# Performance work log

Hardware: AMD Instinct MI355X
Metric: run time of the kernel (lower is better)

## Reference

```python
import jax, jax.numpy as jnp
import numpy as np

B, C, W, H = 1024, 1, 128, 128
NUM_IDS = 64
MARGIN = 0.3


def setup_inputs() -> dict:
    key = jax.random.key(0)
    k1, k2 = jax.random.split(key)
    inputs = jax.random.normal(k1, (B, C, W, H), dtype=jnp.float32)
    targets = jax.random.randint(k2, (B,), 0, NUM_IDS, dtype=jnp.int32)
    return {"inputs": inputs, "targets": targets}


def _dc_align(anchor, other):
    # Batched cross-attention alignment (DCModuleOptimized assumption):
    # modi = softmax(anchor @ other^T / sqrt(h)) @ other, per sample.
    h = anchor.shape[-1]
    scale = 1.0 / jnp.sqrt(jnp.asarray(h, anchor.dtype))
    att = jax.nn.softmax(jnp.einsum('bij,bkj->bik', anchor, other) * scale, axis=-1)
    return jnp.einsum('bik,bkj->bij', att, other)


def reference(inputs, targets):
    b, c, w, h = inputs.shape
    x = inputs.reshape(b, -1)                      # (n, d); requires c == 1 downstream
    n = b
    # Pairwise Euclidean distances, stable clamp as in torch code
    sq = jnp.sum(x * x, axis=1)                    # (n,)
    dist = sq[:, None] + sq[None, :] - 2.0 * (x @ x.T)
    dist = jnp.sqrt(jnp.clip(dist, 1e-12, None))   # (n, n)
    mask = targets[:, None] == targets[None, :]    # (n, n) same-identity mask
    # Vectorized hard mining (replaces the per-row Python loop)
    NEG = jnp.asarray(-1e30, dist.dtype)
    POS = jnp.asarray(1e30, dist.dtype)
    hp_idx = jnp.argmax(jnp.where(mask, dist, NEG), axis=1)   # hardest positive per row
    hn_idx = jnp.argmin(jnp.where(mask, POS, dist), axis=1)   # hardest negative per row
    anchor = x.reshape(b, w, h)
    h_pos = anchor[hp_idx]                         # (b, w, h) gathered hard positives
    h_neg = anchor[hn_idx]                         # (b, w, h) gathered hard negatives
    # DC module applied over the whole batch at once
    modi_pos = _dc_align(anchor, h_pos)
    modi_neg = _dc_align(anchor, h_neg)
    dap = anchor.reshape(b, -1) - modi_pos.reshape(b, -1)
    dan = anchor.reshape(b, -1) - modi_neg.reshape(b, -1)
    dist_ap = jnp.sqrt(jnp.sum(dap * dap, axis=1))
    dist_an = jnp.sqrt(jnp.sum(dan * dan, axis=1))
    # MarginRankingLoss with y = 1: mean(relu(dist_ap - dist_an + margin))
    loss = jnp.mean(jax.nn.relu(dist_ap - dist_an + MARGIN))
    return loss
```

## Files before the change

### kernel.cpp

```cpp
#include <hip/hip_runtime.h>
#include <stdint.h>

#define NSAMP 1024
#define D 16384
#define WH 128
#define MARGIN 0.3f
#define KS 8
#define KSUB (D / KS)
#define SCALE 0.08838834764831845f
#define RSCALE 11.313708498984761f

typedef unsigned int uint;
typedef unsigned short ushort_t;

typedef __attribute__((ext_vector_type(8))) short bf16x8;
typedef __attribute__((ext_vector_type(4))) float f32x4;

__device__ __forceinline__ float bf2f(unsigned short b) {
    return __uint_as_float(((uint)b) << 16);
}
__device__ __forceinline__ unsigned short f2bf(float f) {
    uint u = __float_as_uint(f);
    u += 0x7fffu + ((u >> 16) & 1u);
    return (unsigned short)(u >> 16);
}
__device__ __forceinline__ void gload_lds16(const void* g, void* l) {
    __builtin_amdgcn_global_load_lds(
        (const __attribute__((address_space(1))) uint32_t*)g,
        (__attribute__((address_space(3))) uint32_t*)l, 16, 0, 0);
}
__device__ __forceinline__ bf16x8 bf8_half(bf16x8 v) {
    union { bf16x8 b; uint u[4]; } c;
    c.b = v;
    c.u[0] -= 0x00800080u; c.u[1] -= 0x00800080u;
    c.u[2] -= 0x00800080u; c.u[3] -= 0x00800080u;
    return c.b;
}
__device__ __forceinline__ int lds_off(int row, int col) {
    return row * 256 + ((((col >> 3) ^ (row & 15)) << 4) | ((col & 7) << 1));
}

__global__ __launch_bounds__(256) void k_norms_split(const float* __restrict__ x,
                                                     float* __restrict__ sq,
                                                     ushort_t* __restrict__ xhi,
                                                     ushort_t* __restrict__ xlo) {
    int b = blockIdx.x;
    int tid = threadIdx.x;
    const float* xr = x + (size_t)b * D;
    ushort_t* hr = xhi + (size_t)b * D;
    ushort_t* lr = xlo + (size_t)b * D;
    float s = 0.f;
    #pragma unroll
    for (int m = 0; m < 16; ++m) {
        int e = m * 1024 + tid * 4;
        float4 v = *(const float4*)(xr + e);
        s += v.x * v.x + v.y * v.y + v.z * v.z + v.w * v.w;
        ushort4 h, l;
        h.x = f2bf(v.x); l.x = f2bf(v.x - bf2f(h.x));
        h.y = f2bf(v.y); l.y = f2bf(v.y - bf2f(h.y));
        h.z = f2bf(v.z); l.z = f2bf(v.z - bf2f(h.z));
        h.w = f2bf(v.w); l.w = f2bf(v.w - bf2f(h.w));
        *(ushort4*)(hr + e) = h;
        *(ushort4*)(lr + e) = l;
    }
    for (int off = 32; off; off >>= 1) s += __shfl_down(s, off, 64);
    __shared__ float red[4];
    if ((tid & 63) == 0) red[tid >> 6] = s;
    __syncthreads();
    if (tid == 0) sq[b] = red[0] + red[1] + red[2] + red[3];
}

__global__ __launch_bounds__(256) void k_gram_mfma(const ushort_t* __restrict__ xhi,
                                                   const ushort_t* __restrict__ xlo,
                                                   float* __restrict__ Gp) {
    int lin = blockIdx.x + 8 * blockIdx.y + 64 * blockIdx.z;
    int ks = lin & 7, bi = (lin >> 3) & 7, bj = lin >> 6;
    int i0 = bi * 128, j0 = bj * 128;
    int tid = threadIdx.x;
    int w = tid >> 6, lane = tid & 63;
    int wm = w & 1, wn = w >> 1;
    int quad = lane >> 4, m16 = lane & 15;
    int srow = lane >> 2, sseg = lane & 3;

    __shared__ __align__(16) ushort_t Ahi_s[128 * 32];
    __shared__ __align__(16) ushort_t Bhi_s[128 * 32];
    __shared__ __align__(16) ushort_t Blo_s[128 * 32];

    f32x4 acc[4][4];
    #pragma unroll
    for (int ii = 0; ii < 4; ++ii)
        #pragma unroll
        for (int jj = 0; jj < 4; ++jj)
            acc[ii][jj] = (f32x4){0.f, 0.f, 0.f, 0.f};

    const size_t Abase = (size_t)i0 * D;
    const size_t Bbase = (size_t)j0 * D;

    for (int kb = 0; kb < KSUB / 32; ++kb) {
        int k0 = ks * KSUB + kb * 32;
        #pragma unroll
        for (int c = 0; c < 2; ++c) {
            int r = w * 32 + c * 16 + srow;
            size_t go = (size_t)r * D + k0 + sseg * 8;
            int lo = (w * 32 + c * 16) * 32;
            gload_lds16(xhi + Abase + go, &Ahi_s[lo]);
            gload_lds16(xhi + Bbase + go, &Bhi_s[lo]);
            gload_lds16(xlo + Bbase + go, &Blo_s[lo]);
        }
        __syncthreads();

        bf16x8 ah[4], bh[4], bl[4];
        #pragma unroll
        for (int ii = 0; ii < 4; ++ii) {
            int ar = wm * 64 + ii * 16 + m16;
            ah[ii] = *(const bf16x8*)&Ahi_s[ar * 32 + quad * 8];
        }
        #pragma unroll
        for (int jj = 0; jj < 4; ++jj) {
            int br = wn * 64 + jj * 16 + m16;
            bh[jj] = *(const bf16x8*)&Bhi_s[br * 32 + quad * 8];
            bl[jj] = *(const bf16x8*)&Blo_s[br * 32 + quad * 8];
        }
        #pragma unroll
        for (int ii = 0; ii < 4; ++ii) {
            bf16x8 ahh = bf8_half(ah[ii]);
            #pragma unroll
            for (int jj = 0; jj < 4; ++jj) {
                acc[ii][jj] = __builtin_amdgcn_mfma_f32_16x16x32_bf16(ahh, bh[jj], acc[ii][jj], 0, 0, 0);
                acc[ii][jj] = __builtin_amdgcn_mfma_f32_16x16x32_bf16(ah[ii], bl[jj], acc[ii][jj], 0, 0, 0);
            }
        }
        __syncthreads();
    }

    float* Gb = Gp + (size_t)ks * NSAMP * NSAMP;
    #pragma unroll
    for (int ii = 0; ii < 4; ++ii)
        #pragma unroll
        for (int jj = 0; jj < 4; ++jj) {
            int rg = i0 + wm * 64 + ii * 16 + quad * 4;
            int cg = j0 + wn * 64 + jj * 16 + m16;
            #pragma unroll
            for (int r = 0; r < 4; ++r)
                Gb[(size_t)(rg + r) * NSAMP + cg] = acc[ii][jj][r];
        }
}

__global__ __launch_bounds__(256) void k_fold_sym(const float* __restrict__ Gp,
                                                  float* __restrict__ G) {
    int J = blockIdx.x, I = blockIdx.y;
    int t = threadIdx.x;
    int r = t >> 4, c4 = (t & 15) * 4;
    __shared__ float TJ[64][65];
    float4 sIJ[4];
    #pragma unroll
    for (int rr = 0; rr < 4; ++rr) {
        int row = rr * 16 + r;
        size_t oIJ = (size_t)(I * 64 + row) * NSAMP + J * 64 + c4;
        size_t oJI = (size_t)(J * 64 + row) * NSAMP + I * 64 + c4;
        float4 a = {0.f, 0.f, 0.f, 0.f}, bb = {0.f, 0.f, 0.f, 0.f};
        #pragma unroll
        for (int p = 0; p < KS; ++p) {
            float4 v = *(const float4*)(Gp + (size_t)p * NSAMP * NSAMP + oIJ);
            float4 w = *(const float4*)(Gp + (size_t)p * NSAMP * NSAMP + oJI);
            a.x += v.x; a.y += v.y; a.z += v.z; a.w += v.w;
            bb.x += w.x; bb.y += w.y; bb.z += w.z; bb.w += w.w;
        }
        sIJ[rr] = a;
        TJ[row][c4 + 0] = bb.x; TJ[row][c4 + 1] = bb.y;
        TJ[row][c4 + 2] = bb.z; TJ[row][c4 + 3] = bb.w;
    }
    __syncthreads();
    #pragma unroll
    for (int rr = 0; rr < 4; ++rr) {
        int row = rr * 16 + r;
        float4 v = sIJ[rr];
        v.x += TJ[c4 + 0][row]; v.y += TJ[c4 + 1][row];
        v.z += TJ[c4 + 2][row]; v.w += TJ[c4 + 3][row];
        *(float4*)(G + (size_t)(I * 64 + row) * NSAMP + J * 64 + c4) = v;
    }
}

__global__ void k_select(const float* __restrict__ G,
                         const float* __restrict__ sq, const int* __restrict__ tgt,
                         int* __restrict__ hp, int* __restrict__ hn,
                         float* __restrict__ dsq) {
    int i = blockIdx.x;
    int tid = threadIdx.x;
    float sqi = sq[i];
    int ti = tgt[i];
    float pv = -3.0e38f; int pj = 0x7FFFFFFF;
    float nv = 3.0e38f;  int nj = 0x7FFFFFFF;
    #pragma unroll
    for (int m = 0; m < 4; ++m) {
        int j = tid + 256 * m;
        float g = G[(size_t)i * NSAMP + j];
        float d2 = sqi + sq[j] - 2.f * g;
        float d = sqrtf(fmaxf(d2, 1e-12f));
        bool same = (tgt[j] == ti);
        float cp = same ? d : -1e30f;
        float cn = same ? 1e30f : d;
        if (cp > pv || (cp == pv && j < pj)) { pv = cp; pj = j; }
        if (cn < nv || (cn == nv && j < nj)) { nv = cn; nj = j; }
    }
    for (int off = 32; off; off >>= 1) {
        float opv = __shfl_down(pv, off, 64); int opj = __shfl_down(pj, off, 64);
        float onv = __shfl_down(nv, off, 64); int onj = __shfl_down(nj, off, 64);
        if (opv > pv || (opv == pv && opj < pj)) { pv = opv; pj = opj; }
        if (onv < nv || (onv == nv && onj < nj)) { nv = onv; nj = onj; }
    }
    __shared__ float spv[4], snv[4];
    __shared__ int spj[4], snj[4];
    if ((tid & 63) == 0) { int wv = tid >> 6; spv[wv] = pv; spj[wv] = pj; snv[wv] = nv; snj[wv] = nj; }
    __syncthreads();
    if (tid == 0) {
        for (int wv = 1; wv < 4; ++wv) {
            if (spv[wv] > pv || (spv[wv] == pv && spj[wv] < pj)) { pv = spv[wv]; pj = spj[wv]; }
            if (snv[wv] < nv || (snv[wv] == nv && snj[wv] < nj)) { nv = snv[wv]; nj = snj[wv]; }
        }
        hp[i] = pj; hn[i] = nj;
        dsq[i] = sqi; dsq[NSAMP + i] = sqi;
    }
}

__global__ __launch_bounds__(256) void k_dc_mfma(const ushort_t* __restrict__ xhi,
                                                 const int* __restrict__ hp,
                                                 const int* __restrict__ hn,
                                                 float* __restrict__ dsq) {
    int b = blockIdx.x;
    int which = blockIdx.y;
    int q = blockIdx.z;
    int oidx = (which == 0) ? hp[b] : hn[b];
    const ushort_t* Ag = xhi + (size_t)b * D;
    const ushort_t* Og = xhi + (size_t)oidx * D;

    __shared__ __align__(16) char smem[32768];

    int tid = threadIdx.x;
    int wv = tid >> 6, lane = tid & 63;
    int quad = lane >> 4, m16 = lane & 15;
    int rt = q * 4 + wv;

    bf16x8 af[4];
    #pragma unroll
    for (int ks = 0; ks < 4; ++ks)
        af[ks] = *(const bf16x8*)(Ag + (rt * 16 + m16) * WH + ks * 32 + quad * 8);

    {
        uint4 stg[8];
        #pragma unroll
        for (int k = 0; k < 8; ++k)
            stg[k] = *(const uint4*)((const char*)Og + (size_t)(tid + 256 * k) * 16);
        #pragma unroll
        for (int k = 0; k < 8; ++k) {
            int g = tid + 256 * k;
            *(uint4*)(smem + lds_off(g >> 4, (g & 15) * 8)) = stg[k];
        }
    }
    __syncthreads();

    f32x4 acc[8];
    #pragma unroll
    for (int ti = 0; ti < 8; ++ti)
        acc[ti] = (f32x4){0.f, 0.f, 0.f, 0.f};
    #pragma unroll
    for (int ks = 0; ks < 4; ++ks) {
        bf16x8 of[8];
        #pragma unroll
        for (int ti = 0; ti < 8; ++ti)
            of[ti] = *(const bf16x8*)(smem + lds_off(ti * 16 + m16, (ks * 4 + quad) * 8));
        #pragma unroll
        for (int ti = 0; ti < 8; ++ti)
            acc[ti] = __builtin_amdgcn_mfma_f32_16x16x32_bf16(of[ti], af[ks], acc[ti], 0, 0, 0);
    }

    int c0 = (tid & 31) * 4, h0 = (tid >> 5) * 16;
    uint4 trd[4][2];
    #pragma unroll
    for (int j = 0; j < 4; ++j)
        #pragma unroll
        for (int k = 0; k < 2; ++k)
            trd[j][k] = *(const uint4*)(smem + lds_off(c0 + j, h0 + 8 * k));
    __syncthreads();

    #pragma unroll
    for (int i = 0; i < 16; ++i) {
        uint v[4];
        #pragma unroll
        for (int j = 0; j < 4; ++j) {
            uint wo = ((const uint*)&trd[j][i >> 3])[(i >> 1) & 3];
            v[j] = (i & 1) ? (wo >> 16) : (wo & 0xffffu);
        }
        uint2 pk;
        pk.x = v[0] | (v[1] << 16);
        pk.y = v[2] | (v[3] << 16);
        *(uint2*)(smem + lds_off(h0 + i, c0)) = pk;
    }

    float tpart = 0.f;
    bf16x8 pf[4];
    {
        float mx = -3.0e38f;
        #pragma unroll
        for (int ti = 0; ti < 8; ++ti)
            #pragma unroll
            for (int r = 0; r < 4; ++r) {
                float s = acc[ti][r] * SCALE;
                acc[ti][r] = s;
                mx = fmaxf(mx, s);
            }
        mx = fmaxf(mx, __shfl_xor(mx, 16, 64));
        mx = fmaxf(mx, __shfl_xor(mx, 32, 64));
        float sum = 0.f, tnum = 0.f;
        #pragma unroll
        for (int ti = 0; ti < 8; ++ti)
            #pragma unroll
            for (int r = 0; r < 4; ++r) {
                float s = acc[ti][r];
                float e = __expf(s - mx);
                acc[ti][r] = e;
                sum += e;
                tnum += s * e;
            }
        sum += __shfl_xor(sum, 16, 64);
        sum += __shfl_xor(sum, 32, 64);
        tnum += __shfl_xor(tnum, 16, 64);
        tnum += __shfl_xor(tnum, 32, 64);
        float inv = 1.f / sum;
        tpart = 0.25f * tnum * inv;

        uint Ep[8][2];
        #pragma unroll
        for (int ti = 0; ti < 8; ++ti) {
            Ep[ti][0] = (uint)f2bf(acc[ti][0] * inv) |
                        ((uint)f2bf(acc[ti][1] * inv) << 16);
            Ep[ti][1] = (uint)f2bf(acc[ti][2] * inv) |
                        ((uint)f2bf(acc[ti][3] * inv) << 16);
        }
        int tih = quad >> 1;
        #pragma unroll
        for (int ks = 0; ks < 4; ++ks) {
            union { uint u[4]; bf16x8 v; } fr;
            #pragma unroll
            for (int k = 0; k < 4; ++k) {
                int src = (((quad << 1) + (k >> 1)) & 3) * 16 + m16;
                int a = __shfl((int)Ep[2 * ks + 0][k & 1], src, 64);
                int bsh = __shfl((int)Ep[2 * ks + 1][k & 1], src, 64);
                fr.u[k] = (uint)((tih == 0) ? a : bsh);
            }
            pf[ks] = fr.v;
        }
    }
    __syncthreads();

    #pragma unroll
    for (int tj = 0; tj < 8; ++tj)
        acc[tj] = (f32x4){0.f, 0.f, 0.f, 0.f};
    #pragma unroll
    for (int ks = 0; ks < 4; ++ks) {
        bf16x8 otf[8];
        #pragma unroll
        for (int tj = 0; tj < 8; ++tj)
            otf[tj] = *(const bf16x8*)(smem + lds_off(tj * 16 + m16, (ks * 4 + quad) * 8));
        #pragma unroll
        for (int tj = 0; tj < 8; ++tj)
            acc[tj] = __builtin_amdgcn_mfma_f32_16x16x32_bf16(pf[ks], otf[tj], acc[tj], 0, 0, 0);
    }

    float m2 = 0.f;
    #pragma unroll
    for (int tj = 0; tj < 8; ++tj)
        #pragma unroll
        for (int r = 0; r < 4; ++r) {
            float mvv = acc[tj][r];
            m2 += mvv * mvv;
        }
    float part = m2 - 2.f * RSCALE * tpart;
    for (int off = 32; off; off >>= 1) part += __shfl_down(part, off, 64);
    if (lane == 0) atomicAdd(&dsq[which * NSAMP + b], part);
}

__global__ void k_loss(const float* __restrict__ dsq, float* __restrict__ out) {
    int tid = threadIdx.x;
    float s = 0.f;
    #pragma unroll
    for (int m = 0; m < 4; ++m) {
        int b = tid + 256 * m;
        float ap = sqrtf(fmaxf(dsq[b], 0.f));
        float an = sqrtf(fmaxf(dsq[NSAMP + b], 0.f));
        s += fmaxf(ap - an + MARGIN, 0.f);
    }
    for (int off = 32; off; off >>= 1) s += __shfl_down(s, off, 64);
    __shared__ float red[4];
    if ((tid & 63) == 0) red[tid >> 6] = s;
    __syncthreads();
    if (tid == 0) out[0] = (red[0] + red[1] + red[2] + red[3]) * (1.f / NSAMP);
}

extern "C" void kernel_launch(void* const* d_in, const int* in_sizes, int n_in,
                              void* d_out, int out_size, void* d_ws, size_t ws_size,
                              hipStream_t stream) {
    const float* x = (const float*)d_in[0];
    const int* tgt = (const int*)d_in[1];
    float* out = (float*)d_out;
    char* ws = (char*)d_ws;

    float* Gp = (float*)ws;
    ushort_t* xhi = (ushort_t*)(ws + (size_t)32 * 1024 * 1024);
    ushort_t* xlo = xhi + (size_t)NSAMP * D;
    float* G = (float*)xlo;
    float* sq = (float*)(ws + (size_t)96 * 1024 * 1024);
    float* dsq = sq + NSAMP;
    int* hp = (int*)(dsq + 2 * NSAMP);
    int* hn = hp + NSAMP;

    k_norms_split<<<NSAMP, 256, 0, stream>>>(x, sq, xhi, xlo);
    k_gram_mfma<<<dim3(8, 8, 8), 256, 0, stream>>>(xhi, xlo, Gp);
    k_fold_sym<<<dim3(16, 16), 256, 0, stream>>>(Gp, G);
    k_select<<<NSAMP, 256, 0, stream>>>(G, sq, tgt, hp, hn, dsq);
    k_dc_mfma<<<dim3(NSAMP, 2, 2), 256, 0, stream>>>(xhi, hp, hn, dsq);
    k_loss<<<1, 256, 0, stream>>>(dsq, out);
}
```

Before: 231.1 us.

## Use bf16-only Gram with margin-flagged fp32 refinement of near-tie selections

Replaces the split hi/lo bf16 Gram, which took two MFMAs per tile, with a single bf16 product. That halves the matrix work and drops the xlo buffer. To keep argmax/argmin correct, rows whose best candidate lies within a margin of other candidates are flagged, and a fix kernel recomputes those distances with an fp32 correction term. It also widens the K-split to 16 when workspace allows, loads 64-wide K chunks, and replaces the symmetric fold with a plain sum. The added select/fix passes and the margin heuristic risk extra cost and missed ties if the bf16 error exceeds the margin.

Result: no change. 228.9 us (-0.9%).

```diff
diff --git a/kernel.cpp b/kernel.cpp
--- a/kernel.cpp
+++ b/kernel.cpp
@@ -5,10 +5,10 @@
 #define D 16384
 #define WH 128
 #define MARGIN 0.3f
-#define KS 8
-#define KSUB (D / KS)
 #define SCALE 0.08838834764831845f
 #define RSCALE 11.313708498984761f
+#define MARG 0.03f
+#define LISTCAP 2048
 
 typedef unsigned int uint;
 typedef unsigned short ushort_t;
@@ -29,39 +29,26 @@
         (const __attribute__((address_space(1))) uint32_t*)g,
         (__attribute__((address_space(3))) uint32_t*)l, 16, 0, 0);
 }
-__device__ __forceinline__ bf16x8 bf8_half(bf16x8 v) {
-    union { bf16x8 b; uint u[4]; } c;
-    c.b = v;
-    c.u[0] -= 0x00800080u; c.u[1] -= 0x00800080u;
-    c.u[2] -= 0x00800080u; c.u[3] -= 0x00800080u;
-    return c.b;
-}
 __device__ __forceinline__ int lds_off(int row, int col) {
     return row * 256 + ((((col >> 3) ^ (row & 15)) << 4) | ((col & 7) << 1));
 }
 
-__global__ __launch_bounds__(256) void k_norms_split(const float* __restrict__ x,
-                                                     float* __restrict__ sq,
-                                                     ushort_t* __restrict__ xhi,
-                                                     ushort_t* __restrict__ xlo) {
+__global__ __launch_bounds__(256) void k_norms_hi(const float* __restrict__ x,
+                                                  float* __restrict__ sq,
+                                                  ushort_t* __restrict__ xhi) {
     int b = blockIdx.x;
     int tid = threadIdx.x;
     const float* xr = x + (size_t)b * D;
     ushort_t* hr = xhi + (size_t)b * D;
-    ushort_t* lr = xlo + (size_t)b * D;
     float s = 0.f;
     #pragma unroll
     for (int m = 0; m < 16; ++m) {
         int e = m * 1024 + tid * 4;
         float4 v = *(const float4*)(xr + e);
         s += v.x * v.x + v.y * v.y + v.z * v.z + v.w * v.w;
-        ushort4 h, l;
-        h.x = f2bf(v.x); l.x = f2bf(v.x - bf2f(h.x));
-        h.y = f2bf(v.y); l.y = f2bf(v.y - bf2f(h.y));
-        h.z = f2bf(v.z); l.z = f2bf(v.z - bf2f(h.z));
-        h.w = f2bf(v.w); l.w = f2bf(v.w - bf2f(h.w));
+        ushort4 h;
+        h.x = f2bf(v.x); h.y = f2bf(v.y); h.z = f2bf(v.z); h.w = f2bf(v.w);
         *(ushort4*)(hr + e) = h;
-        *(ushort4*)(lr + e) = l;
     }
     for (int off = 32; off; off >>= 1) s += __shfl_down(s, off, 64);
     __shared__ float red[4];
@@ -70,11 +57,9 @@
     if (tid == 0) sq[b] = red[0] + red[1] + red[2] + red[3];
 }
 
-__global__ __launch_bounds__(256) void k_gram_mfma(const ushort_t* __restrict__ xhi,
-                                                   const ushort_t* __restrict__ xlo,
-                                                   float* __restrict__ Gp) {
-    int lin = blockIdx.x + 8 * blockIdx.y + 64 * blockIdx.z;
-    int ks = lin & 7, bi = (lin >> 3) & 7, bj = lin >> 6;
+__global__ __launch_bounds__(256) void k_gram_hi(const ushort_t* __restrict__ xhi,
+                                                 float* __restrict__ Gp, int ksub) {
+    int ks = blockIdx.x, bi = blockIdx.y, bj = blockIdx.z;
     int i0 = bi * 128, j0 = bj * 128;
     int tid = threadIdx.x;
     int w = tid >> 6, lane = tid & 63;
@@ -82,9 +67,8 @@
     int quad = lane >> 4, m16 = lane & 15;
     int srow = lane >> 2, sseg = lane & 3;
 
-    __shared__ __align__(16) ushort_t Ahi_s[128 * 32];
-    __shared__ __align__(16) ushort_t Bhi_s[128 * 32];
-    __shared__ __align__(16) ushort_t Blo_s[128 * 32];
+    __shared__ __align__(16) ushort_t A_s[2][128 * 32];
+    __shared__ __align__(16) ushort_t B_s[2][128 * 32];
 
     f32x4 acc[4][4];
     #pragma unroll
@@ -96,39 +80,39 @@
     const size_t Abase = (size_t)i0 * D;
     const size_t Bbase = (size_t)j0 * D;
 
-    for (int kb = 0; kb < KSUB / 32; ++kb) {
-        int k0 = ks * KSUB + kb * 32;
-        #pragma unroll
-        for (int c = 0; c < 2; ++c) {
-            int r = w * 32 + c * 16 + srow;
-            size_t go = (size_t)r * D + k0 + sseg * 8;
-            int lo = (w * 32 + c * 16) * 32;
-            gload_lds16(xhi + Abase + go, &Ahi_s[lo]);
-            gload_lds16(xhi + Bbase + go, &Bhi_s[lo]);
-            gload_lds16(xlo + Bbase + go, &Blo_s[lo]);
+    for (int kb = 0; kb < ksub / 64; ++kb) {
+        int k0 = ks * ksub + kb * 64;
+        #pragma unroll
+        for (int kk = 0; kk < 2; ++kk) {
+            #pragma unroll
+            for (int c = 0; c < 2; ++c) {
+                int r = w * 32 + c * 16 + srow;
+                size_t go = (size_t)r * D + k0 + kk * 32 + sseg * 8;
+                int lo = (w * 32 + c * 16) * 32;
+                gload_lds16(xhi + Abase + go, &A_s[kk][lo]);
+                gload_lds16(xhi + Bbase + go, &B_s[kk][lo]);
+            }
         }
         __syncthreads();
 
-        bf16x8 ah[4], bh[4], bl[4];
-        #pragma unroll
-        for (int ii = 0; ii < 4; ++ii) {
-            int ar = wm * 64 + ii * 16 + m16;
-            ah[ii] = *(const bf16x8*)&Ahi_s[ar * 32 + quad * 8];
-        }
-        #pragma unroll
-        for (int jj = 0; jj < 4; ++jj) {
-            int br = wn * 64 + jj * 16 + m16;
-            bh[jj] = *(const bf16x8*)&Bhi_s[br * 32 + quad * 8];
-            bl[jj] = *(const bf16x8*)&Blo_s[br * 32 + quad * 8];
-        }
-        #pragma unroll
-        for (int ii = 0; ii < 4; ++ii) {
-            bf16x8 ahh = bf8_half(ah[ii]);
+        #pragma unroll
+        for (int kk = 0; kk < 2; ++kk) {
+            bf16x8 ah[4], bh[4];
+            #pragma unroll
+            for (int ii = 0; ii < 4; ++ii) {
+                int ar = wm * 64 + ii * 16 + m16;
+                ah[ii] = *(const bf16x8*)&A_s[kk][ar * 32 + quad * 8];
+            }
             #pragma unroll
             for (int jj = 0; jj < 4; ++jj) {
-                acc[ii][jj] = __builtin_amdgcn_mfma_f32_16x16x32_bf16(ahh, bh[jj], acc[ii][jj], 0, 0, 0);
-                acc[ii][jj] = __builtin_amdgcn_mfma_f32_16x16x32_bf16(ah[ii], bl[jj], acc[ii][jj], 0, 0, 0);
-            }
+                int br = wn * 64 + jj * 16 + m16;
+                bh[jj] = *(const bf16x8*)&B_s[kk][br * 32 + quad * 8];
+            }
+            #pragma unroll
+            for (int ii = 0; ii < 4; ++ii)
+                #pragma unroll
+                for (int jj = 0; jj < 4; ++jj)
+                    acc[ii][jj] = __builtin_amdgcn_mfma_f32_16x16x32_bf16(ah[ii], bh[jj], acc[ii][jj], 0, 0, 0);
         }
         __syncthreads();
     }
@@ -146,58 +130,38 @@
         }
 }
 
-__global__ __launch_bounds__(256) void k_fold_sym(const float* __restrict__ Gp,
-                                                  float* __restrict__ G) {
-    int J = blockIdx.x, I = blockIdx.y;
-    int t = threadIdx.x;
-    int r = t >> 4, c4 = (t & 15) * 4;
-    __shared__ float TJ[64][65];
-    float4 sIJ[4];
-    #pragma unroll
-    for (int rr = 0; rr < 4; ++rr) {
-        int row = rr * 16 + r;
-        size_t oIJ = (size_t)(I * 64 + row) * NSAMP + J * 64 + c4;
-        size_t oJI = (size_t)(J * 64 + row) * NSAMP + I * 64 + c4;
-        float4 a = {0.f, 0.f, 0.f, 0.f}, bb = {0.f, 0.f, 0.f, 0.f};
-        #pragma unroll
-        for (int p = 0; p < KS; ++p) {
-            float4 v = *(const float4*)(Gp + (size_t)p * NSAMP * NSAMP + oIJ);
-            float4 w = *(const float4*)(Gp + (size_t)p * NSAMP * NSAMP + oJI);
-            a.x += v.x; a.y += v.y; a.z += v.z; a.w += v.w;
-            bb.x += w.x; bb.y += w.y; bb.z += w.z; bb.w += w.w;
-        }
-        sIJ[rr] = a;
-        TJ[row][c4 + 0] = bb.x; TJ[row][c4 + 1] = bb.y;
-        TJ[row][c4 + 2] = bb.z; TJ[row][c4 + 3] = bb.w;
-    }
-    __syncthreads();
-    #pragma unroll
-    for (int rr = 0; rr < 4; ++rr) {
-        int row = rr * 16 + r;
-        float4 v = sIJ[rr];
-        v.x += TJ[c4 + 0][row]; v.y += TJ[c4 + 1][row];
-        v.z += TJ[c4 + 2][row]; v.w += TJ[c4 + 3][row];
-        *(float4*)(G + (size_t)(I * 64 + row) * NSAMP + J * 64 + c4) = v;
-    }
-}
-
-__global__ void k_select(const float* __restrict__ G,
-                         const float* __restrict__ sq, const int* __restrict__ tgt,
-                         int* __restrict__ hp, int* __restrict__ hn,
-                         float* __restrict__ dsq) {
+__global__ __launch_bounds__(256) void k_fold(const float* __restrict__ Gp,
+                                              float* __restrict__ G, int nks,
+                                              int* __restrict__ cnt) {
+    if (blockIdx.x == 0 && threadIdx.x == 0) cnt[0] = 0;
+    size_t idx = ((size_t)blockIdx.x * 256 + threadIdx.x) * 4;
+    float4 s = *(const float4*)(Gp + idx);
+    for (int p = 1; p < nks; ++p) {
+        float4 v = *(const float4*)(Gp + (size_t)p * NSAMP * NSAMP + idx);
+        s.x += v.x; s.y += v.y; s.z += v.z; s.w += v.w;
+    }
+    *(float4*)(G + idx) = s;
+}
+
+__global__ void k_select_flag(const float* __restrict__ G,
+                              const float* __restrict__ sq, const int* __restrict__ tgt,
+                              int* __restrict__ hp, int* __restrict__ hn,
+                              float* __restrict__ dsq, float* __restrict__ bestd,
+                              int* __restrict__ list, int* __restrict__ cnt) {
     int i = blockIdx.x;
     int tid = threadIdx.x;
     float sqi = sq[i];
     int ti = tgt[i];
+    float dloc[4]; bool sloc[4];
     float pv = -3.0e38f; int pj = 0x7FFFFFFF;
     float nv = 3.0e38f;  int nj = 0x7FFFFFFF;
     #pragma unroll
     for (int m = 0; m < 4; ++m) {
         int j = tid + 256 * m;
         float g = G[(size_t)i * NSAMP + j];
-        float d2 = sqi + sq[j] - 2.f * g;
-        float d = sqrtf(fmaxf(d2, 1e-12f));
+        float d = sqrtf(fmaxf(sqi + sq[j] - 2.f * g, 1e-12f));
         bool same = (tgt[j] == ti);
+        dloc[m] = d; sloc[m] = same;
         float cp = same ? d : -1e30f;
         float cn = same ? 1e30f : d;
         if (cp > pv || (cp == pv && j < pj)) { pv = cp; pj = j; }
@@ -211,6 +175,8 @@
     }
     __shared__ float spv[4], snv[4];
     __shared__ int spj[4], snj[4];
+    __shared__ float bb[2];
+    __shared__ int cc[2];
     if ((tid & 63) == 0) { int wv = tid >> 6; spv[wv] = pv; spj[wv] = pj; snv[wv] = nv; snj[wv] = nj; }
     __syncthreads();
     if (tid == 0) {
@@ -220,6 +186,100 @@
         }
         hp[i] = pj; hn[i] = nj;
         dsq[i] = sqi; dsq[NSAMP + i] = sqi;
+        bestd[i] = pv; bestd[NSAMP + i] = nv;
+        bb[0] = pv; bb[1] = nv;
+        cc[0] = 0; cc[1] = 0;
+    }
+    __syncthreads();
+    float bp = bb[0], bn = bb[1];
+    int lp = 0, ln = 0;
+    #pragma unroll
+    for (int m = 0; m < 4; ++m) {
+        if (sloc[m] && dloc[m] >= bp - MARG) lp++;
+        if (!sloc[m] && dloc[m] <= bn + MARG) ln++;
+    }
+    if (lp) atomicAdd(&cc[0], lp);
+    if (ln) atomicAdd(&cc[1], ln);
+    __syncthreads();
+    if (tid == 0) {
+        if (cc[0] > 1) { int k = atomicAdd(cnt, 1); if (k < LISTCAP) list[k] = i; }
+        if (cc[1] > 1) { int k = atomicAdd(cnt, 1); if (k < LISTCAP) list[k] = i | (1 << 16); }
+    }
+}
+
+__global__ __launch_bounds__(256) void k_fix(const float* __restrict__ G,
+                                             const float* __restrict__ sq,
+                                             const int* __restrict__ tgt,
+                                             const float* __restrict__ x,
+                                             const ushort_t* __restrict__ xhi,
+                                             const float* __restrict__ bestd,
+                                             const int* __restrict__ list,
+                                             const int* __restrict__ cnt,
+                                             int* __restrict__ hp, int* __restrict__ hn) {
+    int n = cnt[0]; if (n > LISTCAP) n = LISTCAP;
+    int tid = threadIdx.x;
+    __shared__ int cand[32];
+    __shared__ int ncand;
+    __shared__ float bred[4];
+    for (int e = blockIdx.x; e < n; e += gridDim.x) {
+        int ent = list[e];
+        int i = ent & 0xffff, type = ent >> 16;
+        if (tid == 0) ncand = 0;
+        __syncthreads();
+        float bd = bestd[type * NSAMP + i];
+        float sqi = sq[i];
+        int ti = tgt[i];
+        #pragma unroll
+        for (int m = 0; m < 4; ++m) {
+            int j = tid + 256 * m;
+            float g = G[(size_t)i * NSAMP + j];
+            float d = sqrtf(fmaxf(sqi + sq[j] - 2.f * g, 1e-12f));
+            bool same = (tgt[j] == ti);
+            bool fl = (type == 0) ? (same && d >= bd - MARG)
+                                  : (!same && d <= bd + MARG);
+            if (fl) { int k = atomicAdd(&ncand, 1); if (k < 32) cand[k] = j; }
+        }
+        __syncthreads();
+        int nc = ncand < 32 ? ncand : 32;
+        float bestv = (type == 0) ? -3.0e38f : 3.0e38f;
+        int bestj = 0x7FFFFFFF;
+        const float* xi = x + (size_t)i * D;
+        const ushort_t* hi = xhi + (size_t)i * D;
+        for (int c = 0; c < nc; ++c) {
+            int j = cand[c];
+            const float* xj = x + (size_t)j * D;
+            const ushort_t* hj = xhi + (size_t)j * D;
+            float corr = 0.f;
+            #pragma unroll
+            for (int m = 0; m < 16; ++m) {
+                int k = m * 1024 + tid * 4;
+                float4 xa = *(const float4*)(xi + k);
+                float4 xb = *(const float4*)(xj + k);
+                ushort4 ha = *(const ushort4*)(hi + k);
+                ushort4 hb = *(const ushort4*)(hj + k);
+                float a0 = bf2f(ha.x), a1 = bf2f(ha.y), a2 = bf2f(ha.z), a3 = bf2f(ha.w);
+                float b0 = bf2f(hb.x), b1 = bf2f(hb.y), b2 = bf2f(hb.z), b3 = bf2f(hb.w);
+                corr += a0 * (xb.x - b0) + (xa.x - a0) * b0;
+                corr += a1 * (xb.y - b1) + (xa.y - a1) * b1;
+                corr += a2 * (xb.z - b2) + (xa.z - a2) * b2;
+                corr += a3 * (xb.w - b3) + (xa.w - a3) * b3;
+            }
+            for (int off = 32; off; off >>= 1) corr += __shfl_down(corr, off, 64);
+            if ((tid & 63) == 0) bred[tid >> 6] = corr;
+            __syncthreads();
+            float cs = bred[0] + bred[1] + bred[2] + bred[3];
+            float g = G[(size_t)i * NSAMP + j];
+            float d2 = sqi + sq[j] - 2.f * (g + cs);
+            float d = sqrtf(fmaxf(d2, 1e-12f));
+            if (type == 0) {
+                if (d > bestv || (d == bestv && j < bestj)) { bestv = d; bestj = j; }
+            } else {
+                if (d < bestv || (d == bestv && j < bestj)) { bestv = d; bestj = j; }
+            }
+            __syncthreads();
+        }
+        if (tid == 0 && nc > 0) { if (type == 0) hp[i] = bestj; else hn[i] = bestj; }
+        __syncthreads();
     }
 }
 
@@ -405,19 +465,27 @@
     float* out = (float*)d_out;
     char* ws = (char*)d_ws;
 
+    const size_t XB = (size_t)NSAMP * D * 2;
+    const size_t GB1 = (size_t)NSAMP * NSAMP * 4;
+    int nks = (ws_size >= 16 * GB1 + XB + GB1 + (size_t)65536) ? 16 : 8;
+
     float* Gp = (float*)ws;
-    ushort_t* xhi = (ushort_t*)(ws + (size_t)32 * 1024 * 1024);
-    ushort_t* xlo = xhi + (size_t)NSAMP * D;
-    float* G = (float*)xlo;
-    float* sq = (float*)(ws + (size_t)96 * 1024 * 1024);
+    ushort_t* xhi = (ushort_t*)(ws + nks * GB1);
+    float* G = (float*)(ws + nks * GB1 + XB);
+    char* tail = ws + nks * GB1 + XB + GB1;
+    float* sq = (float*)tail;
     float* dsq = sq + NSAMP;
-    int* hp = (int*)(dsq + 2 * NSAMP);
+    float* bestd = dsq + 2 * NSAMP;
+    int* hp = (int*)(bestd + 2 * NSAMP);
     int* hn = hp + NSAMP;
-
-    k_norms_split<<<NSAMP, 256, 0, stream>>>(x, sq, xhi, xlo);
-    k_gram_mfma<<<dim3(8, 8, 8), 256, 0, stream>>>(xhi, xlo, Gp);
-    k_fold_sym<<<dim3(16, 16), 256, 0, stream>>>(Gp, G);
-    k_select<<<NSAMP, 256, 0, stream>>>(G, sq, tgt, hp, hn, dsq);
+    int* list = hn + NSAMP;
+    int* cnt = list + LISTCAP;
+
+    k_norms_hi<<<NSAMP, 256, 0, stream>>>(x, sq, xhi);
+    k_gram_hi<<<dim3(nks, 8, 8), 256, 0, stream>>>(xhi, Gp, D / nks);
+    k_fold<<<NSAMP, 256, 0, stream>>>(Gp, G, nks, cnt);
+    k_select_flag<<<NSAMP, 256, 0, stream>>>(G, sq, tgt, hp, hn, dsq, bestd, list, cnt);
+    k_fix<<<64, 256, 0, stream>>>(G, sq, tgt, x, xhi, bestd, list, cnt, hp, hn);
     k_dc_mfma<<<dim3(NSAMP, 2, 2), 256, 0, stream>>>(xhi, hp, hn, dsq);
     k_loss<<<1, 256, 0, stream>>>(dsq, out);
 }
```
